# Kernel tuning notes

Hardware: AMD Instinct MI355X
Metric: run time of the kernel (lower is better)

Reference implementation:

```python
import jax, jax.numpy as jnp
import numpy as np

NUM_CAPSULE = 32
DIM_CAPSULE = 16
NUM_ITERATIONS = 3


def squash(v):
    # v: [B, O, F]; squash along last dim
    norm = jnp.linalg.norm(v, axis=-1, keepdims=True)
    mag = norm * norm
    return v / norm * mag / (1.0 + mag)


def setup_inputs() -> dict:
    key = jax.random.key(0)
    k1, k2 = jax.random.split(key)
    B, L, H = 128, 512, 256
    O, F = NUM_CAPSULE, DIM_CAPSULE
    x = jax.random.normal(k1, (B, L, H), dtype=jnp.float32)
    # xavier_normal for [1, H, O*F]: std = sqrt(2 / (H + O*F))
    std = float(np.sqrt(2.0 / (H + O * F)))
    W = jax.random.normal(k2, (1, H, O * F), dtype=jnp.float32) * std
    return {"x": x, "W": W}


def reference(x, W):
    B, I, H = x.shape
    O, F = NUM_CAPSULE, DIM_CAPSULE
    # u: [B, I, O*F] -> [B, O, I, F]
    u = jnp.matmul(x, W)  # broadcasts shared W [1,H,O*F]
    u = u.reshape(B, I, O, F).transpose(0, 2, 1, 3)
    b = jnp.zeros((B, O, I), dtype=u.dtype)
    v = None
    for _ in range(NUM_ITERATIONS):
        c = jax.nn.softmax(b, axis=1)            # softmax over output capsules O
        v = jnp.einsum('boi,boif->bof', c, u)    # weighted aggregation
        v = squash(v)
        b = jnp.einsum('bof,boif->boi', v, u)    # agreement logits
    return v
```

## Files before the change

### kernel.cpp

```cpp
#include <hip/hip_runtime.h>

#define BB 128
#define II 512
#define HH 256
#define OO 32
#define FF 16
#define OF 512
#define CI 64
#define NP 8
#define X16STR 264
#define CSTRI 68
#define C2STR 36

typedef __attribute__((ext_vector_type(8))) short short8;
typedef __attribute__((ext_vector_type(4))) float floatx4;

__device__ __forceinline__ ushort f2bf(float f) {
  unsigned u = __float_as_uint(f);
  u += 0x7FFFu + ((u >> 16) & 1u);
  return (ushort)(u >> 16);
}
__device__ __forceinline__ float bf2f(ushort u) {
  return __uint_as_float(((unsigned)u) << 16);
}

__global__ __launch_bounds__(256) void k_xsum(
    const float* __restrict__ x, float* __restrict__ xsum_part) {
  int t = threadIdx.x;
  int blk = blockIdx.x;
  int b = blk >> 3, ch = blk & 7;
  const float* xp = x + ((size_t)b * II + (size_t)ch * 64) * HH + t;
  float a = 0.f;
#pragma unroll 8
  for (int i = 0; i < 64; ++i) a += xp[(size_t)i * HH];
  xsum_part[(size_t)blk * HH + t] = a;
}

__global__ __launch_bounds__(512) void k_v1(
    const float* __restrict__ xsum_part, const float* __restrict__ W,
    float* __restrict__ v) {
  __shared__ float xs[HH];
  int t = threadIdx.x;
  int b = blockIdx.x;
  if (t < HH) {
    float a = 0.f;
#pragma unroll
    for (int ch = 0; ch < 8; ++ch) a += xsum_part[((size_t)b * 8 + ch) * HH + t];
    xs[t] = a;
  }
  __syncthreads();
  float acc = 0.f;
#pragma unroll 4
  for (int h = 0; h < HH; ++h)
    acc += xs[h] * W[(size_t)h * OF + t];
  acc *= (1.0f / 32.0f);
  float n2 = acc * acc;
#pragma unroll
  for (int mask = 1; mask < 16; mask <<= 1) n2 += __shfl_xor(n2, mask);
  float scale = sqrtf(n2) / (1.f + n2);
  v[(size_t)b * OF + t] = acc * scale;
}

__global__ __launch_bounds__(256) void k_wv(
    const float* __restrict__ W, const float* __restrict__ v,
    ushort* __restrict__ wvT16) {
  __shared__ float Ws[64 * 17];
  __shared__ float vsb[BB * 17];
  int t = threadIdx.x;
  int blk = blockIdx.x;
  int o = blk & 31, hq = blk >> 5;
#pragma unroll
  for (int jj = 0; jj < 4; ++jj) {
    int idx = jj * 256 + t;
    int hl = idx >> 4, f = idx & 15;
    Ws[hl * 17 + f] = W[((size_t)(hq * 64 + hl)) * OF + o * FF + f];
  }
#pragma unroll
  for (int jj = 0; jj < 8; ++jj) {
    int idx = jj * 256 + t;
    int b = idx >> 4, f = idx & 15;
    vsb[b * 17 + f] = v[((size_t)b * OO + o) * FF + f];
  }
  __syncthreads();
  int hl = t & 63, bq = t >> 6;
  for (int bb = 0; bb < BB; bb += 4) {
    int b = bb + bq;
    float acc = 0.f;
#pragma unroll
    for (int f = 0; f < FF; ++f) acc += Ws[hl * 17 + f] * vsb[b * 17 + f];
    wvT16[((size_t)b * OO + o) * HH + hq * 64 + hl] = f2bf(acc);
  }
}

__global__ __launch_bounds__(256, 3) void k_route(
    const float* __restrict__ x, const ushort* __restrict__ wvT16,
    ushort* __restrict__ cxp16) {
  __shared__ ushort x16[CI * X16STR];
  __shared__ float cs[OO * CSTRI];
  __shared__ float c2[CI * C2STR];
  int t = threadIdx.x;
  int blk = blockIdx.x;
  int b = blk >> 3, p = blk & 7;
  int lane = t & 63, wvid = t >> 6;
  int l16 = lane & 15, quad = lane >> 4;

  int mt = wvid & 1;
  short8 afrag[8];
  {
    const ushort* wvp = wvT16 + ((size_t)b * OO + mt * 16 + l16) * HH + quad * 8;
#pragma unroll
    for (int ks = 0; ks < 8; ++ks)
      afrag[ks] = *(const short8*)(wvp + ks * 32);
  }

  {
    const float* xg = x + ((size_t)b * II + (size_t)p * CI) * HH;
#pragma unroll
    for (int j = 0; j < 16; ++j) {
      int idx = j * 256 + t;
      int row = idx >> 6, c4 = idx & 63;
      float4 v4 = *(const float4*)(xg + (size_t)row * HH + c4 * 4);
      ushort4 u;
      u.x = f2bf(v4.x); u.y = f2bf(v4.y); u.z = f2bf(v4.z); u.w = f2bf(v4.w);
      *(ushort4*)&x16[row * X16STR + c4 * 4] = u;
    }
  }
  __syncthreads();

  {
    int nt0 = wvid >> 1;
#pragma unroll
    for (int rep = 0; rep < 2; ++rep) {
      int nt = nt0 + rep * 2;
      floatx4 acc = {0.f, 0.f, 0.f, 0.f};
#pragma unroll
      for (int ks = 0; ks < 8; ++ks) {
        short8 bfrag = *(const short8*)&x16[(nt * 16 + l16) * X16STR + ks * 32 + quad * 8];
        acc = __builtin_amdgcn_mfma_f32_16x16x32_bf16(afrag[ks], bfrag, acc, 0, 0, 0);
      }
#pragma unroll
      for (int r = 0; r < 4; ++r)
        cs[(mt * 16 + quad * 4 + r) * CSTRI + nt * 16 + l16] = acc[r];
    }
  }
  __syncthreads();

  if (wvid == 0) {
    float lg[32];
    float m = -1e30f;
#pragma unroll
    for (int o = 0; o < 32; ++o) { lg[o] = cs[o * CSTRI + lane]; m = fmaxf(m, lg[o]); }
    float s = 0.f;
#pragma unroll
    for (int o = 0; o < 32; ++o) { lg[o] = __expf(lg[o] - m); s += lg[o]; }
    float inv = 1.f / s;
#pragma unroll
    for (int k = 0; k < 8; ++k) {
      float4 cc = make_float4(lg[4 * k] * inv, lg[4 * k + 1] * inv,
                              lg[4 * k + 2] * inv, lg[4 * k + 3] * inv);
      *(float4*)&c2[lane * C2STR + 4 * k] = cc;
    }
  }
  __syncthreads();

  {
    int hg = t & 63, og3 = t >> 6;
    int h0 = hg * 4, o0 = og3 * 8;
    float4 a4[8];
#pragma unroll
    for (int j = 0; j < 8; ++j) a4[j] = make_float4(0.f, 0.f, 0.f, 0.f);
#pragma unroll 4
    for (int i = 0; i < CI; ++i) {
      ushort4 xu = *(const ushort4*)&x16[i * X16STR + h0];
      float4 x4 = make_float4(bf2f(xu.x), bf2f(xu.y), bf2f(xu.z), bf2f(xu.w));
      float4 c0 = *(const float4*)&c2[i * C2STR + o0];
      float4 c1 = *(const float4*)&c2[i * C2STR + o0 + 4];
      float cv[8] = {c0.x, c0.y, c0.z, c0.w, c1.x, c1.y, c1.z, c1.w};
#pragma unroll
      for (int j = 0; j < 8; ++j) {
        a4[j].x += cv[j] * x4.x;
        a4[j].y += cv[j] * x4.y;
        a4[j].z += cv[j] * x4.z;
        a4[j].w += cv[j] * x4.w;
      }
    }
    ushort* outp = cxp16 + ((size_t)blk * OO + o0) * HH + h0;
#pragma unroll
    for (int j = 0; j < 8; ++j) {
      ushort4 u;
      u.x = f2bf(a4[j].x); u.y = f2bf(a4[j].y);
      u.z = f2bf(a4[j].z); u.w = f2bf(a4[j].w);
      *(ushort4*)&outp[(size_t)j * HH] = u;
    }
  }
}

__global__ __launch_bounds__(256) void k_v2(
    const ushort* __restrict__ cxp16, const float* __restrict__ W,
    float* __restrict__ v, float* __restrict__ out, int final_) {
  __shared__ float cxs[HH];
  __shared__ float red[4][16];
  int t = threadIdx.x;
  int blk = blockIdx.x;
  int b = blk >> 5, o = blk & 31;
  {
    const ushort* cp = cxp16 + (((size_t)b * NP) * OO + o) * HH + t;
    float a = 0.f;
#pragma unroll
    for (int p = 0; p < NP; ++p) a += bf2f(cp[(size_t)p * OO * HH]);
    cxs[t] = a;
  }
  __syncthreads();
  int f = t & 15, hq = t >> 4;
  const float* wp = W + (size_t)hq * 16 * OF + o * FF + f;
  float acc = 0.f;
#pragma unroll
  for (int j = 0; j < 16; ++j)
    acc += cxs[hq * 16 + j] * wp[(size_t)j * OF];
  acc += __shfl_xor(acc, 16);
  acc += __shfl_xor(acc, 32);
  if ((t & 63) < 16) red[t >> 6][f] = acc;
  __syncthreads();
  if (t < 16) {
    float a = red[0][t] + red[1][t] + red[2][t] + red[3][t];
    float n2 = a * a;
#pragma unroll
    for (int mask = 1; mask < 16; mask <<= 1) n2 += __shfl_xor(n2, mask);
    float scale = sqrtf(n2) / (1.f + n2);
    float res = a * scale;
    if (final_) out[(size_t)blk * FF + t] = res;
    else v[(size_t)blk * FF + t] = res;
  }
}

extern "C" void kernel_launch(void* const* d_in, const int* in_sizes, int n_in,
                              void* d_out, int out_size, void* d_ws, size_t ws_size,
                              hipStream_t stream) {
  const float* x = (const float*)d_in[0];
  const float* W = (const float*)d_in[1];
  float* out = (float*)d_out;
  float* ws = (float*)d_ws;
  float*  xsum_part = ws;
  float*  v     = ws + 262144;
  ushort* wvT16 = (ushort*)(ws + 327680);
  ushort* cxp16 = (ushort*)(ws + 851968);

  k_xsum<<<BB * 8, 256, 0, stream>>>(x, xsum_part);
  k_v1<<<BB, 512, 0, stream>>>(xsum_part, W, v);
  for (int it = 0; it < 2; ++it) {
    k_wv<<<128, 256, 0, stream>>>(W, v, wvT16);
    k_route<<<BB * NP, 256, 0, stream>>>(x, wvT16, cxp16);
    k_v2<<<BB * OO, 256, 0, stream>>>(cxp16, W, v, out, it == 1);
  }
}
```

Measured before the change: 189.8 us.

## Precompute bf16 x and x-transpose once, use MFMA for routing aggregation, fuse wv

A new prep kernel reads x once to produce the bf16 copy, a bf16 transposed copy and the partial sums, so each routing pass stops re-reading and converting the fp32 x. The routing kernel now computes logits with MFMA straight from global bf16 data, does the softmax over capsules with cross-lane shuffles, and replaces the scalar FMA aggregation loop with MFMA on the transposed x. The W·v product is folded into k_v1 and k_v2, which removes the separate k_wv launch. In exchange it writes and reads two extra bf16 copies of x in the workspace and stores the softmax weights as bf16.

```diff
diff --git a/kernel.cpp b/kernel.cpp
--- a/kernel.cpp
+++ b/kernel.cpp
@@ -8,9 +8,8 @@
 #define OF 512
 #define CI 64
 #define NP 8
-#define X16STR 264
-#define CSTRI 68
-#define C2STR 36
+#define XTSTR 260
+#define CSTR 72
 
 typedef __attribute__((ext_vector_type(8))) short short8;
 typedef __attribute__((ext_vector_type(4))) float floatx4;
@@ -24,22 +23,54 @@
   return __uint_as_float(((unsigned)u) << 16);
 }
 
-__global__ __launch_bounds__(256) void k_xsum(
-    const float* __restrict__ x, float* __restrict__ xsum_part) {
+__global__ __launch_bounds__(256) void k_prep(
+    const float* __restrict__ x, ushort* __restrict__ x16,
+    ushort* __restrict__ xT16, float* __restrict__ xsum_part) {
+  __shared__ ushort xt[CI * XTSTR];
+  __shared__ float4 red[4][64];
   int t = threadIdx.x;
   int blk = blockIdx.x;
-  int b = blk >> 3, ch = blk & 7;
-  const float* xp = x + ((size_t)b * II + (size_t)ch * 64) * HH + t;
-  float a = 0.f;
-#pragma unroll 8
-  for (int i = 0; i < 64; ++i) a += xp[(size_t)i * HH];
-  xsum_part[(size_t)blk * HH + t] = a;
+  int c4 = t & 63, grp = t >> 6;
+  const float* xg = x + (size_t)blk * CI * HH;
+  ushort* x16g = x16 + (size_t)blk * CI * HH;
+  float4 sum = make_float4(0.f, 0.f, 0.f, 0.f);
+#pragma unroll
+  for (int j = 0; j < 16; ++j) {
+    int row = j * 4 + grp;
+    float4 v4 = *(const float4*)(xg + (size_t)row * HH + c4 * 4);
+    sum.x += v4.x; sum.y += v4.y; sum.z += v4.z; sum.w += v4.w;
+    ushort4 u;
+    u.x = f2bf(v4.x); u.y = f2bf(v4.y); u.z = f2bf(v4.z); u.w = f2bf(v4.w);
+    *(ushort4*)&xt[row * XTSTR + c4 * 4] = u;
+    *(ushort4*)&x16g[(size_t)row * HH + c4 * 4] = u;
+  }
+  red[grp][c4] = sum;
+  __syncthreads();
+  if (t < 64) {
+    float4 s = red[0][t];
+    float4 s1 = red[1][t], s2 = red[2][t], s3 = red[3][t];
+    s.x += s1.x + s2.x + s3.x; s.y += s1.y + s2.y + s3.y;
+    s.z += s1.z + s2.z + s3.z; s.w += s1.w + s2.w + s3.w;
+    *(float4*)&xsum_part[(size_t)blk * HH + t * 4] = s;
+  }
+  ushort* xtg = xT16 + (size_t)blk * HH * CI + (size_t)t * CI;
+#pragma unroll
+  for (int ch = 0; ch < 8; ++ch) {
+    ushort4 a, bq;
+    a.x = xt[(ch * 8 + 0) * XTSTR + t]; a.y = xt[(ch * 8 + 1) * XTSTR + t];
+    a.z = xt[(ch * 8 + 2) * XTSTR + t]; a.w = xt[(ch * 8 + 3) * XTSTR + t];
+    bq.x = xt[(ch * 8 + 4) * XTSTR + t]; bq.y = xt[(ch * 8 + 5) * XTSTR + t];
+    bq.z = xt[(ch * 8 + 6) * XTSTR + t]; bq.w = xt[(ch * 8 + 7) * XTSTR + t];
+    *(ushort4*)(xtg + ch * 8) = a;
+    *(ushort4*)(xtg + ch * 8 + 4) = bq;
+  }
 }
 
 __global__ __launch_bounds__(512) void k_v1(
     const float* __restrict__ xsum_part, const float* __restrict__ W,
-    float* __restrict__ v) {
+    ushort* __restrict__ wvT16) {
   __shared__ float xs[HH];
+  __shared__ float vs2[OF];
   int t = threadIdx.x;
   int b = blockIdx.x;
   if (t < HH) {
@@ -58,148 +89,98 @@
 #pragma unroll
   for (int mask = 1; mask < 16; mask <<= 1) n2 += __shfl_xor(n2, mask);
   float scale = sqrtf(n2) / (1.f + n2);
-  v[(size_t)b * OF + t] = acc * scale;
-}
-
-__global__ __launch_bounds__(256) void k_wv(
-    const float* __restrict__ W, const float* __restrict__ v,
-    ushort* __restrict__ wvT16) {
-  __shared__ float Ws[64 * 17];
-  __shared__ float vsb[BB * 17];
+  vs2[t] = acc * scale;
+  __syncthreads();
+  int h = t & 255, og = t >> 8;
+  const float* wb = W + (size_t)h * OF;
+#pragma unroll 2
+  for (int j = 0; j < 16; ++j) {
+    int o = og * 16 + j;
+    const float4* wp = (const float4*)(wb + o * FF);
+    const float4* vp = (const float4*)(vs2 + o * FF);
+    float a = 0.f;
+#pragma unroll
+    for (int q = 0; q < 4; ++q) {
+      float4 w4 = wp[q], v4 = vp[q];
+      a += w4.x * v4.x + w4.y * v4.y + w4.z * v4.z + w4.w * v4.w;
+    }
+    wvT16[((size_t)b * OO + o) * HH + h] = f2bf(a);
+  }
+}
+
+__global__ __launch_bounds__(256, 4) void k_route(
+    const ushort* __restrict__ x16, const ushort* __restrict__ xT16,
+    const ushort* __restrict__ wvT16, ushort* __restrict__ cxp16) {
+  __shared__ ushort c2[OO * CSTR];
   int t = threadIdx.x;
   int blk = blockIdx.x;
-  int o = blk & 31, hq = blk >> 5;
-#pragma unroll
-  for (int jj = 0; jj < 4; ++jj) {
-    int idx = jj * 256 + t;
-    int hl = idx >> 4, f = idx & 15;
-    Ws[hl * 17 + f] = W[((size_t)(hq * 64 + hl)) * OF + o * FF + f];
-  }
-#pragma unroll
-  for (int jj = 0; jj < 8; ++jj) {
-    int idx = jj * 256 + t;
-    int b = idx >> 4, f = idx & 15;
-    vsb[b * 17 + f] = v[((size_t)b * OO + o) * FF + f];
-  }
-  __syncthreads();
-  int hl = t & 63, bq = t >> 6;
-  for (int bb = 0; bb < BB; bb += 4) {
-    int b = bb + bq;
-    float acc = 0.f;
-#pragma unroll
-    for (int f = 0; f < FF; ++f) acc += Ws[hl * 17 + f] * vsb[b * 17 + f];
-    wvT16[((size_t)b * OO + o) * HH + hq * 64 + hl] = f2bf(acc);
-  }
-}
-
-__global__ __launch_bounds__(256, 3) void k_route(
-    const float* __restrict__ x, const ushort* __restrict__ wvT16,
-    ushort* __restrict__ cxp16) {
-  __shared__ ushort x16[CI * X16STR];
-  __shared__ float cs[OO * CSTRI];
-  __shared__ float c2[CI * C2STR];
-  int t = threadIdx.x;
-  int blk = blockIdx.x;
-  int b = blk >> 3, p = blk & 7;
-  int lane = t & 63, wvid = t >> 6;
+  int b = blk >> 3;
+  int lane = t & 63, w = t >> 6;
   int l16 = lane & 15, quad = lane >> 4;
 
-  int mt = wvid & 1;
-  short8 afrag[8];
-  {
-    const ushort* wvp = wvT16 + ((size_t)b * OO + mt * 16 + l16) * HH + quad * 8;
-#pragma unroll
-    for (int ks = 0; ks < 8; ++ks)
-      afrag[ks] = *(const short8*)(wvp + ks * 32);
-  }
-
-  {
-    const float* xg = x + ((size_t)b * II + (size_t)p * CI) * HH;
-#pragma unroll
-    for (int j = 0; j < 16; ++j) {
-      int idx = j * 256 + t;
-      int row = idx >> 6, c4 = idx & 63;
-      float4 v4 = *(const float4*)(xg + (size_t)row * HH + c4 * 4);
-      ushort4 u;
-      u.x = f2bf(v4.x); u.y = f2bf(v4.y); u.z = f2bf(v4.z); u.w = f2bf(v4.w);
-      *(ushort4*)&x16[row * X16STR + c4 * 4] = u;
-    }
-  }
-  __syncthreads();
-
-  {
-    int nt0 = wvid >> 1;
-#pragma unroll
-    for (int rep = 0; rep < 2; ++rep) {
-      int nt = nt0 + rep * 2;
-      floatx4 acc = {0.f, 0.f, 0.f, 0.f};
-#pragma unroll
-      for (int ks = 0; ks < 8; ++ks) {
-        short8 bfrag = *(const short8*)&x16[(nt * 16 + l16) * X16STR + ks * 32 + quad * 8];
-        acc = __builtin_amdgcn_mfma_f32_16x16x32_bf16(afrag[ks], bfrag, acc, 0, 0, 0);
-      }
-#pragma unroll
-      for (int r = 0; r < 4; ++r)
-        cs[(mt * 16 + quad * 4 + r) * CSTRI + nt * 16 + l16] = acc[r];
-    }
-  }
-  __syncthreads();
-
-  if (wvid == 0) {
-    float lg[32];
-    float m = -1e30f;
-#pragma unroll
-    for (int o = 0; o < 32; ++o) { lg[o] = cs[o * CSTRI + lane]; m = fmaxf(m, lg[o]); }
-    float s = 0.f;
-#pragma unroll
-    for (int o = 0; o < 32; ++o) { lg[o] = __expf(lg[o] - m); s += lg[o]; }
+  const ushort* xrow = x16 + ((size_t)blk * CI + w * 16 + l16) * HH + quad * 8;
+  const ushort* wv0 = wvT16 + ((size_t)b * OO + l16) * HH + quad * 8;
+  const ushort* wv1 = wv0 + 16 * HH;
+  floatx4 acc0 = {0.f, 0.f, 0.f, 0.f}, acc1 = {0.f, 0.f, 0.f, 0.f};
+#pragma unroll
+  for (int ks = 0; ks < 8; ++ks) {
+    short8 af = *(const short8*)(xrow + ks * 32);
+    short8 b0 = *(const short8*)(wv0 + ks * 32);
+    short8 b1 = *(const short8*)(wv1 + ks * 32);
+    acc0 = __builtin_amdgcn_mfma_f32_16x16x32_bf16(af, b0, acc0, 0, 0, 0);
+    acc1 = __builtin_amdgcn_mfma_f32_16x16x32_bf16(af, b1, acc1, 0, 0, 0);
+  }
+#pragma unroll
+  for (int r = 0; r < 4; ++r) {
+    float a0 = acc0[r], a1 = acc1[r];
+    float m = fmaxf(a0, a1);
+#pragma unroll
+    for (int mask = 1; mask < 16; mask <<= 1) m = fmaxf(m, __shfl_xor(m, mask));
+    float e0 = __expf(a0 - m), e1 = __expf(a1 - m);
+    float s = e0 + e1;
+#pragma unroll
+    for (int mask = 1; mask < 16; mask <<= 1) s += __shfl_xor(s, mask);
     float inv = 1.f / s;
-#pragma unroll
-    for (int k = 0; k < 8; ++k) {
-      float4 cc = make_float4(lg[4 * k] * inv, lg[4 * k + 1] * inv,
-                              lg[4 * k + 2] * inv, lg[4 * k + 3] * inv);
-      *(float4*)&c2[lane * C2STR + 4 * k] = cc;
-    }
-  }
-  __syncthreads();
-
-  {
-    int hg = t & 63, og3 = t >> 6;
-    int h0 = hg * 4, o0 = og3 * 8;
-    float4 a4[8];
-#pragma unroll
-    for (int j = 0; j < 8; ++j) a4[j] = make_float4(0.f, 0.f, 0.f, 0.f);
-#pragma unroll 4
-    for (int i = 0; i < CI; ++i) {
-      ushort4 xu = *(const ushort4*)&x16[i * X16STR + h0];
-      float4 x4 = make_float4(bf2f(xu.x), bf2f(xu.y), bf2f(xu.z), bf2f(xu.w));
-      float4 c0 = *(const float4*)&c2[i * C2STR + o0];
-      float4 c1 = *(const float4*)&c2[i * C2STR + o0 + 4];
-      float cv[8] = {c0.x, c0.y, c0.z, c0.w, c1.x, c1.y, c1.z, c1.w};
-#pragma unroll
-      for (int j = 0; j < 8; ++j) {
-        a4[j].x += cv[j] * x4.x;
-        a4[j].y += cv[j] * x4.y;
-        a4[j].z += cv[j] * x4.z;
-        a4[j].w += cv[j] * x4.w;
-      }
-    }
-    ushort* outp = cxp16 + ((size_t)blk * OO + o0) * HH + h0;
-#pragma unroll
-    for (int j = 0; j < 8; ++j) {
-      ushort4 u;
-      u.x = f2bf(a4[j].x); u.y = f2bf(a4[j].y);
-      u.z = f2bf(a4[j].z); u.w = f2bf(a4[j].w);
-      *(ushort4*)&outp[(size_t)j * HH] = u;
+    int il = w * 16 + quad * 4 + r;
+    c2[l16 * CSTR + il] = f2bf(e0 * inv);
+    c2[(16 + l16) * CSTR + il] = f2bf(e1 * inv);
+  }
+  __syncthreads();
+
+  short8 caf[2][2];
+#pragma unroll
+  for (int mt = 0; mt < 2; ++mt)
+#pragma unroll
+    for (int ks = 0; ks < 2; ++ks)
+      caf[mt][ks] = *(const short8*)&c2[(mt * 16 + l16) * CSTR + ks * 32 + quad * 8];
+  const ushort* xtp = xT16 + (size_t)blk * HH * CI;
+  ushort* outp0 = cxp16 + (size_t)blk * OO * HH;
+#pragma unroll
+  for (int hi = 0; hi < 4; ++hi) {
+    int ht = w * 4 + hi;
+    const ushort* xtr = xtp + (size_t)(ht * 16 + l16) * CI + quad * 8;
+    floatx4 d0 = {0.f, 0.f, 0.f, 0.f}, d1 = {0.f, 0.f, 0.f, 0.f};
+#pragma unroll
+    for (int ks = 0; ks < 2; ++ks) {
+      short8 bf = *(const short8*)(xtr + ks * 32);
+      d0 = __builtin_amdgcn_mfma_f32_16x16x32_bf16(caf[0][ks], bf, d0, 0, 0, 0);
+      d1 = __builtin_amdgcn_mfma_f32_16x16x32_bf16(caf[1][ks], bf, d1, 0, 0, 0);
+    }
+    ushort* outp = outp0 + ht * 16 + l16;
+#pragma unroll
+    for (int r = 0; r < 4; ++r) {
+      outp[(size_t)(quad * 4 + r) * HH] = f2bf(d0[r]);
+      outp[(size_t)(16 + quad * 4 + r) * HH] = f2bf(d1[r]);
     }
   }
 }
 
 __global__ __launch_bounds__(256) void k_v2(
     const ushort* __restrict__ cxp16, const float* __restrict__ W,
-    float* __restrict__ v, float* __restrict__ out, int final_) {
+    ushort* __restrict__ wvT16, float* __restrict__ out, int final_) {
   __shared__ float cxs[HH];
   __shared__ float red[4][16];
+  __shared__ float vres[FF];
   int t = threadIdx.x;
   int blk = blockIdx.x;
   int b = blk >> 5, o = blk & 31;
@@ -229,7 +210,19 @@
     float scale = sqrtf(n2) / (1.f + n2);
     float res = a * scale;
     if (final_) out[(size_t)blk * FF + t] = res;
-    else v[(size_t)blk * FF + t] = res;
+    else vres[t] = res;
+  }
+  if (!final_) {
+    __syncthreads();
+    const float4* wq = (const float4*)(W + (size_t)t * OF + o * FF);
+    const float4* vp = (const float4*)vres;
+    float a = 0.f;
+#pragma unroll
+    for (int q = 0; q < 4; ++q) {
+      float4 w4 = wq[q], v4 = vp[q];
+      a += w4.x * v4.x + w4.y * v4.y + w4.z * v4.z + w4.w * v4.w;
+    }
+    wvT16[((size_t)b * OO + o) * HH + t] = f2bf(a);
   }
 }
 
@@ -241,15 +234,15 @@
   float* out = (float*)d_out;
   float* ws = (float*)d_ws;
   float*  xsum_part = ws;
-  float*  v     = ws + 262144;
-  ushort* wvT16 = (ushort*)(ws + 327680);
-  ushort* cxp16 = (ushort*)(ws + 851968);
-
-  k_xsum<<<BB * 8, 256, 0, stream>>>(x, xsum_part);
-  k_v1<<<BB, 512, 0, stream>>>(xsum_part, W, v);
+  ushort* wvT16 = (ushort*)(ws + 262144);
+  ushort* x16   = (ushort*)(ws + 786432);
+  ushort* xT16  = (ushort*)(ws + 9175040);
+  ushort* cxp16 = (ushort*)(ws + 17563648);
+
+  k_prep<<<BB * NP, 256, 0, stream>>>(x, x16, xT16, xsum_part);
+  k_v1<<<BB, 512, 0, stream>>>(xsum_part, W, wvT16);
   for (int it = 0; it < 2; ++it) {
-    k_wv<<<128, 256, 0, stream>>>(W, v, wvT16);
-    k_route<<<BB * NP, 256, 0, stream>>>(x, wvT16, cxp16);
-    k_v2<<<BB * OO, 256, 0, stream>>>(cxp16, W, v, out, it == 1);
-  }
-}
+    k_route<<<BB * NP, 256, 0, stream>>>(x16, xT16, wvT16, cxp16);
+    k_v2<<<BB * OO, 256, 0, stream>>>(cxp16, W, wvT16, out, it == 1);
+  }
+}
```

Result: slower. 213.0 us (+12.2%).
